# Performance work log

Measured on AMD Instinct MI355X. Metric: run time of the kernel, lower is better.

The kernel has to match this reference:

```python
import jax, jax.numpy as jnp
import numpy as np

N_ATOMS = 100000
N_BONDS = 200001
ATOM_FDIM = 39
BOND_FDIM = 11
MAX_NB = 6
HIDDEN = 256
DEPTH = 6
N_MOLS = 2000
ATOMS_PER_MOL = N_ATOMS // N_MOLS


def setup_inputs() -> dict:
    key = jax.random.key(0)
    ks = jax.random.split(key, 8)
    fatoms = jax.random.uniform(ks[0], (N_ATOMS, ATOM_FDIM), dtype=jnp.float32)
    fbonds = jax.random.uniform(ks[1], (N_BONDS, ATOM_FDIM + BOND_FDIM), dtype=jnp.float32)
    agraph = jax.random.randint(ks[2], (N_ATOMS, MAX_NB), 0, N_BONDS, dtype=jnp.int32)
    bgraph = jax.random.randint(ks[3], (N_BONDS, MAX_NB), 0, N_BONDS, dtype=jnp.int32)
    starts = jnp.arange(N_MOLS, dtype=jnp.int32) * ATOMS_PER_MOL
    scope = jnp.stack([starts, jnp.full((N_MOLS,), ATOMS_PER_MOL, jnp.int32)], axis=1)
    s = 1.0 / np.sqrt(HIDDEN)
    W_i = jax.random.normal(ks[4], (HIDDEN, ATOM_FDIM + BOND_FDIM), dtype=jnp.float32) * s
    W_h = jax.random.normal(ks[5], (HIDDEN, HIDDEN), dtype=jnp.float32) * s
    W_o = jax.random.normal(ks[6], (HIDDEN, ATOM_FDIM + HIDDEN), dtype=jnp.float32) * s
    b_o = jax.random.normal(ks[7], (HIDDEN,), dtype=jnp.float32) * s
    return {"fatoms": fatoms, "fbonds": fbonds, "agraph": agraph,
            "bgraph": bgraph, "scope": scope, "W_i": W_i, "W_h": W_h,
            "W_o": W_o, "b_o": b_o}


def reference(fatoms, fbonds, agraph, bgraph, scope, W_i, W_h, W_o, b_o):
    # Initial bond messages: Linear (no bias) + ReLU
    binput = fbonds @ W_i.T                      # [B_bonds, H]
    message = jax.nn.relu(binput)
    # depth-1 rounds of gather -> sum over MAX_NB neighbors -> Linear -> ReLU + residual
    for _ in range(DEPTH - 1):
        nei = message[bgraph].sum(axis=1)        # [B_bonds, H]
        message = jax.nn.relu(binput + nei @ W_h.T)
    # Atom readout
    nei = message[agraph].sum(axis=1)            # [N_atoms, H]
    ainput = jnp.concatenate([fatoms, nei], axis=1)
    atom_hiddens = jax.nn.relu(ainput @ W_o.T + b_o)
    # Scope mean pooling: equal-size contiguous segments -> reshape-mean
    n_mols = scope.shape[0]
    mol_vecs = atom_hiddens.reshape(n_mols, -1, atom_hiddens.shape[-1]).mean(axis=1)
    return mol_vecs
```

## Files before the change

### kernel.cpp

```cpp
#include <hip/hip_runtime.h>
#include <hip/hip_bf16.h>

#define NB 200001
#define NA 100000
#define HID 256
#define AF 39
#define BFD 50
#define MAXNB 6
#define NMOL 2000
#define APM 50
#define KPAD 320
#define BM 64

typedef __attribute__((ext_vector_type(8))) unsigned short ushort8;
typedef __attribute__((ext_vector_type(8))) short short8;
typedef __attribute__((ext_vector_type(4))) unsigned short u16x4;
typedef __attribute__((ext_vector_type(4))) float f32x4;

__device__ __forceinline__ unsigned short f2b(float f) {
  __hip_bfloat16 h = __float2bfloat16(f);
  return *reinterpret_cast<unsigned short*>(&h);
}
__device__ __forceinline__ float b2f(unsigned short u) {
  union { unsigned int i; float f; } v; v.i = ((unsigned int)u) << 16; return v.f;
}

__global__ void prep_wc(const float* __restrict__ Wi, const float* __restrict__ Wh,
                        unsigned short* __restrict__ WcB) {
  int i = blockIdx.x * 256 + threadIdx.x;
  if (i >= HID * KPAD) return;
  int n = i / KPAD, k = i % KPAD;
  float v = 0.f;
  if (k < BFD) v = Wi[n * BFD + k];
  else if (k >= 64) v = Wh[n * HID + (k - 64)];
  WcB[i] = f2b(v);
}
__global__ void prep_wo(const float* __restrict__ Wo, unsigned short* __restrict__ WoP) {
  int i = blockIdx.x * 256 + threadIdx.x;
  if (i >= HID * KPAD) return;
  int n = i / KPAD, k = i % KPAD;
  float v = 0.f;
  if (k < AF) v = Wo[n * (AF + HID) + k];
  else if (k >= 64) v = Wo[n * (AF + HID) + AF + (k - 64)];
  WoP[i] = f2b(v);
}
__global__ void prep_fb(const float* __restrict__ fbonds, unsigned short* __restrict__ fbpad) {
  int i = blockIdx.x * 256 + threadIdx.x;
  if (i >= NB * 8) return;
  const int bond = i >> 3;
  const int c0 = (i & 7) * 8;
  ushort8 o;
  #pragma unroll
  for (int e = 0; e < 8; ++e) {
    const int c = c0 + e;
    o[e] = f2b(c < BFD ? fbonds[(size_t)bond * BFD + c] : 0.f);
  }
  *reinterpret_cast<ushort8*>(fbpad + (size_t)bond * 64 + c0) = o;
}

template <bool PREPPED>
__device__ __forceinline__ void stage_feat64(unsigned short (*As)[KPAD], int t, int b0,
                                             int nrows_total,
                                             const float* __restrict__ f32src, int f32dim, int realdim,
                                             const unsigned short* __restrict__ padsrc) {
  const int rs = t >> 3, csl = t & 7;
  #pragma unroll
  for (int it = 0; it < 2; ++it) {
    const int r = it * 32 + rs;
    const int row = b0 + r;
    const int c0 = csl * 8;
    ushort8 o;
    #pragma unroll
    for (int e = 0; e < 8; ++e) o[e] = 0;
    if (PREPPED) {
      if (row < nrows_total) o = *reinterpret_cast<const ushort8*>(padsrc + (size_t)row * 64 + c0);
    } else {
      #pragma unroll
      for (int e = 0; e < 8; ++e) {
        const int c = c0 + e;
        if (row < nrows_total && c < realdim) o[e] = f2b(f32src[(size_t)row * f32dim + c]);
      }
    }
    *reinterpret_cast<ushort8*>(&As[r][c0 ^ ((r & 7) << 3)]) = o;
  }
}

#define GLOAD(dst, ROW)                                                              \
  {                                                                                  \
    const int bond_ = b0 + (ROW);                                                    \
    const int* bg_ = graph + (size_t)(bond_ < nrows_total ? bond_ : 0) * MAXNB;      \
    _Pragma("unroll")                                                                \
    for (int j = 0; j < MAXNB; ++j)                                                  \
      dst[j] = *reinterpret_cast<const u16x4*>(msg_in + (size_t)bg_[j] * HID + c0);  \
  }
#define GCONSUME(src, ROW)                                                           \
  {                                                                                  \
    float acc_[4] = {0.f, 0.f, 0.f, 0.f};                                            \
    _Pragma("unroll")                                                                \
    for (int j = 0; j < MAXNB; ++j) {                                                \
      _Pragma("unroll")                                                              \
      for (int e = 0; e < 4; ++e) acc_[e] += b2f(src[j][e]);                         \
    }                                                                                \
    u16x4 o_;                                                                        \
    _Pragma("unroll")                                                                \
    for (int e = 0; e < 4; ++e) o_[e] = f2b(acc_[e]);                                \
    const int r_ = (ROW);                                                            \
    const int cc_ = 64 + c0;                                                         \
    *reinterpret_cast<u16x4*>(&As[r_][cc_ ^ ((r_ & 7) << 3)]) = o_;                  \
  }

__device__ __forceinline__ void gather_rows64(unsigned short (*As)[KPAD],
                                              const int* __restrict__ graph,
                                              int t, int b0, int nrows_total,
                                              const unsigned short* __restrict__ msg_in) {
  const int w = t >> 6;
  const int lane = t & 63;
  const int c0 = lane * 4;
  u16x4 va[MAXNB], vb[MAXNB], vc[MAXNB], vd[MAXNB];
  GLOAD(va, 0 * 4 + w);
  GLOAD(vb, 1 * 4 + w);
  GLOAD(vc, 2 * 4 + w);
  #pragma unroll
  for (int i4 = 0; i4 < 16; i4 += 4) {
    { const int it = i4 + 0; if (it + 3 < 16) GLOAD(vd, (it + 3) * 4 + w); GCONSUME(va, it * 4 + w); }
    { const int it = i4 + 1; if (it + 3 < 16) GLOAD(va, (it + 3) * 4 + w); GCONSUME(vb, it * 4 + w); }
    { const int it = i4 + 2; if (it + 3 < 16) GLOAD(vb, (it + 3) * 4 + w); GCONSUME(vc, it * 4 + w); }
    { const int it = i4 + 3; if (it + 3 < 16) GLOAD(vc, (it + 3) * 4 + w); GCONSUME(vd, it * 4 + w); }
  }
}

template <bool PREPPED>
__global__ __launch_bounds__(256, 4) void init_kernel(
    const float* __restrict__ fbonds, const unsigned short* __restrict__ fbpad,
    const unsigned short* __restrict__ WcB, unsigned short* __restrict__ msg0) {
  __shared__ unsigned short As[BM][KPAD];
  const int t = threadIdx.x;
  const int b0 = blockIdx.x * BM;

  stage_feat64<PREPPED>(As, t, b0, NB, fbonds, BFD, BFD, fbpad);
  __syncthreads();

  const int w = t >> 6, lane = t & 63, lr = lane & 15, lg = lane >> 4;
  f32x4 acc[4][4];
  #pragma unroll
  for (int i = 0; i < 4; ++i)
    #pragma unroll
    for (int j = 0; j < 4; ++j) acc[i][j] = f32x4{0.f, 0.f, 0.f, 0.f};

  const unsigned short* wb[4];
  #pragma unroll
  for (int fn = 0; fn < 4; ++fn) wb[fn] = WcB + (size_t)(w * 64 + fn * 16 + lr) * KPAD;

  #pragma unroll
  for (int ks = 0; ks < 2; ++ks) {
    const int kb = ks * 32 + lg * 8;
    short8 a[4], b[4];
    #pragma unroll
    for (int fm = 0; fm < 4; ++fm) {
      const int m = fm * 16 + lr;
      a[fm] = *reinterpret_cast<const short8*>(&As[m][kb ^ ((m & 7) << 3)]);
    }
    #pragma unroll
    for (int fn = 0; fn < 4; ++fn)
      b[fn] = *reinterpret_cast<const short8*>(wb[fn] + kb);
    #pragma unroll
    for (int fm = 0; fm < 4; ++fm)
      #pragma unroll
      for (int fn = 0; fn < 4; ++fn)
        acc[fm][fn] = __builtin_amdgcn_mfma_f32_16x16x32_bf16(a[fm], b[fn], acc[fm][fn], 0, 0, 0);
  }

  #pragma unroll
  for (int fm = 0; fm < 4; ++fm)
    #pragma unroll
    for (int r = 0; r < 4; ++r) {
      const int m = fm * 16 + lg * 4 + r;
      const int bond = b0 + m;
      if (bond < NB) {
        #pragma unroll
        for (int fn = 0; fn < 4; ++fn) {
          const int col = w * 64 + fn * 16 + lr;
          msg0[(size_t)bond * HID + col] = f2b(fmaxf(acc[fm][fn][r], 0.f));
        }
      }
    }
}

template <bool PREPPED>
__global__ __launch_bounds__(256, 4) void round_kernel(
    const unsigned short* __restrict__ msg_in, unsigned short* __restrict__ msg_out,
    const float* __restrict__ fbonds, const unsigned short* __restrict__ fbpad,
    const unsigned short* __restrict__ WcB, const int* __restrict__ bgraph) {
  __shared__ unsigned short As[BM][KPAD];
  const int t = threadIdx.x;
  const int b0 = blockIdx.x * BM;

  stage_feat64<PREPPED>(As, t, b0, NB, fbonds, BFD, BFD, fbpad);
  gather_rows64(As, bgraph, t, b0, NB, msg_in);
  __syncthreads();

  const int w = t >> 6, lane = t & 63, lr = lane & 15, lg = lane >> 4;
  f32x4 acc[4][4];
  #pragma unroll
  for (int i = 0; i < 4; ++i)
    #pragma unroll
    for (int j = 0; j < 4; ++j) acc[i][j] = f32x4{0.f, 0.f, 0.f, 0.f};

  const unsigned short* wb[4];
  #pragma unroll
  for (int fn = 0; fn < 4; ++fn) wb[fn] = WcB + (size_t)(w * 64 + fn * 16 + lr) * KPAD;

  for (int kstep = 0; kstep < 5; ++kstep) {
    #pragma unroll
    for (int ks = 0; ks < 2; ++ks) {
      const int kb = ks * 32 + lg * 8;
      const int kA = kstep * 64 + kb;
      short8 a[4], b[4];
      #pragma unroll
      for (int fm = 0; fm < 4; ++fm) {
        const int m = fm * 16 + lr;
        a[fm] = *reinterpret_cast<const short8*>(&As[m][kA ^ ((m & 7) << 3)]);
      }
      #pragma unroll
      for (int fn = 0; fn < 4; ++fn)
        b[fn] = *reinterpret_cast<const short8*>(wb[fn] + kstep * 64 + kb);
      #pragma unroll
      for (int fm = 0; fm < 4; ++fm)
        #pragma unroll
        for (int fn = 0; fn < 4; ++fn)
          acc[fm][fn] = __builtin_amdgcn_mfma_f32_16x16x32_bf16(a[fm], b[fn], acc[fm][fn], 0, 0, 0);
    }
  }

  #pragma unroll
  for (int fm = 0; fm < 4; ++fm)
    #pragma unroll
    for (int r = 0; r < 4; ++r) {
      const int m = fm * 16 + lg * 4 + r;
      const int bond = b0 + m;
      if (bond < NB) {
        #pragma unroll
        for (int fn = 0; fn < 4; ++fn) {
          const int col = w * 64 + fn * 16 + lr;
          __builtin_nontemporal_store(f2b(fmaxf(acc[fm][fn][r], 0.f)),
                                      &msg_out[(size_t)bond * HID + col]);
        }
      }
    }
}

__global__ __launch_bounds__(256, 4) void readout_kernel(
    const unsigned short* __restrict__ msg_in, const float* __restrict__ fatoms,
    const unsigned short* __restrict__ WoP, const float* __restrict__ b_o,
    const int* __restrict__ agraph, float* __restrict__ atomh) {
  __shared__ unsigned short As[BM][KPAD];
  const int t = threadIdx.x;
  const int a0 = blockIdx.x * BM;

  stage_feat64<false>(As, t, a0, NA, fatoms, AF, AF, nullptr);
  gather_rows64(As, agraph, t, a0, NA, msg_in);
  __syncthreads();

  const int w = t >> 6, lane = t & 63, lr = lane & 15, lg = lane >> 4;
  f32x4 acc[4][4];
  #pragma unroll
  for (int i = 0; i < 4; ++i)
    #pragma unroll
    for (int j = 0; j < 4; ++j) acc[i][j] = f32x4{0.f, 0.f, 0.f, 0.f};

  const unsigned short* wb[4];
  #pragma unroll
  for (int fn = 0; fn < 4; ++fn) wb[fn] = WoP + (size_t)(w * 64 + fn * 16 + lr) * KPAD;

  for (int kstep = 0; kstep < 5; ++kstep) {
    #pragma unroll
    for (int ks = 0; ks < 2; ++ks) {
      const int kb = ks * 32 + lg * 8;
      const int kA = kstep * 64 + kb;
      short8 a[4], b[4];
      #pragma unroll
      for (int fm = 0; fm < 4; ++fm) {
        const int m = fm * 16 + lr;
        a[fm] = *reinterpret_cast<const short8*>(&As[m][kA ^ ((m & 7) << 3)]);
      }
      #pragma unroll
      for (int fn = 0; fn < 4; ++fn)
        b[fn] = *reinterpret_cast<const short8*>(wb[fn] + kstep * 64 + kb);
      #pragma unroll
      for (int fm = 0; fm < 4; ++fm)
        #pragma unroll
        for (int fn = 0; fn < 4; ++fn)
          acc[fm][fn] = __builtin_amdgcn_mfma_f32_16x16x32_bf16(a[fm], b[fn], acc[fm][fn], 0, 0, 0);
    }
  }

  #pragma unroll
  for (int fm = 0; fm < 4; ++fm)
    #pragma unroll
    for (int r = 0; r < 4; ++r) {
      const int m = fm * 16 + lg * 4 + r;
      const int atom = a0 + m;
      if (atom < NA) {
        #pragma unroll
        for (int fn = 0; fn < 4; ++fn) {
          const int col = w * 64 + fn * 16 + lr;
          const float v = acc[fm][fn][r] + b_o[col];
          __builtin_nontemporal_store(fmaxf(v, 0.f), &atomh[(size_t)atom * HID + col]);
        }
      }
    }
}

__global__ __launch_bounds__(256) void pool_kernel(const float* __restrict__ atomh,
                                                   float* __restrict__ out) {
  const int mol = blockIdx.x;
  const int t = threadIdx.x;
  const float* base = atomh + (size_t)mol * APM * HID + t;
  float s = 0.f;
  #pragma unroll 5
  for (int i = 0; i < APM; ++i) s += base[(size_t)i * HID];
  out[(size_t)mol * HID + t] = s * (1.f / APM);
}

extern "C" void kernel_launch(void* const* d_in, const int* in_sizes, int n_in,
                              void* d_out, int out_size, void* d_ws, size_t ws_size,
                              hipStream_t stream) {
  const float* fatoms = (const float*)d_in[0];
  const float* fbonds = (const float*)d_in[1];
  const int* agraph = (const int*)d_in[2];
  const int* bgraph = (const int*)d_in[3];
  const float* W_i = (const float*)d_in[5];
  const float* W_h = (const float*)d_in[6];
  const float* W_o = (const float*)d_in[7];
  const float* b_o = (const float*)d_in[8];

  char* ws = (char*)d_ws;
  size_t off = 0;
  auto alloc = [&](size_t bytes) {
    void* p = ws + off;
    off += (bytes + 255) & ~(size_t)255;
    return p;
  };
  unsigned short* msgA = (unsigned short*)alloc((size_t)NB * HID * 2);
  unsigned short* msgB = (unsigned short*)alloc((size_t)NB * HID * 2);
  unsigned short* WcB = (unsigned short*)alloc((size_t)HID * KPAD * 2);
  unsigned short* WoP = (unsigned short*)alloc((size_t)HID * KPAD * 2);
  const size_t base_need = off;
  unsigned short* fbpad = (unsigned short*)alloc((size_t)NB * 64 * 2);
  const size_t fb_need = off;
  float* atomh = (float*)msgA;

  if (ws_size < base_need) return;
  const bool prepped = (ws_size >= fb_need);

  prep_wc<<<(HID * KPAD + 255) / 256, 256, 0, stream>>>(W_i, W_h, WcB);
  prep_wo<<<(HID * KPAD + 255) / 256, 256, 0, stream>>>(W_o, WoP);
  if (prepped)
    prep_fb<<<(NB * 8 + 255) / 256, 256, 0, stream>>>(fbonds, fbpad);

  const int nblk_b = (NB + BM - 1) / BM;
  if (prepped)
    init_kernel<true><<<nblk_b, 256, 0, stream>>>(fbonds, fbpad, WcB, msgA);
  else
    init_kernel<false><<<nblk_b, 256, 0, stream>>>(fbonds, fbpad, WcB, msgA);

  unsigned short* src = msgA;
  unsigned short* dst = msgB;
  for (int d = 0; d < 5; ++d) {
    if (prepped)
      round_kernel<true><<<nblk_b, 256, 0, stream>>>(src, dst, fbonds, fbpad, WcB, bgraph);
    else
      round_kernel<false><<<nblk_b, 256, 0, stream>>>(src, dst, fbonds, fbpad, WcB, bgraph);
    unsigned short* tmp = src; src = dst; dst = tmp;
  }

  const int nblk_a = (NA + BM - 1) / BM;
  readout_kernel<<<nblk_a, 256, 0, stream>>>(src, fatoms, WoP, b_o, agraph, atomh);
  pool_kernel<<<NMOL, 256, 0, stream>>>(atomh, (float*)d_out);
}
```

Measured before the change: 959.1 us.

## Quantize bond messages to 8-bit with per-row scales to halve gather traffic

Stores each round's bond messages as unsigned 8-bit values with a per-bond float scale instead of bf16. The GEMM epilogue now does a cross-wave row max through shared memory to compute the scale. Gathers dequantize on the fly, halving the bytes pulled by the random-access neighbour gather that dominates each round. This adds extra syncs and reductions in the epilogue and loses precision relative to bf16. The workspace layout also changes: fbpad now aliases the atomh buffer and the unprepped fallback path is removed.

```diff
diff --git a/kernel.cpp b/kernel.cpp
--- a/kernel.cpp
+++ b/kernel.cpp
@@ -58,10 +58,8 @@
   *reinterpret_cast<ushort8*>(fbpad + (size_t)bond * 64 + c0) = o;
 }
 
-template <bool PREPPED>
 __device__ __forceinline__ void stage_feat64(unsigned short (*As)[KPAD], int t, int b0,
                                              int nrows_total,
-                                             const float* __restrict__ f32src, int f32dim, int realdim,
                                              const unsigned short* __restrict__ padsrc) {
   const int rs = t >> 3, csl = t & 7;
   #pragma unroll
@@ -72,72 +70,135 @@
     ushort8 o;
     #pragma unroll
     for (int e = 0; e < 8; ++e) o[e] = 0;
-    if (PREPPED) {
-      if (row < nrows_total) o = *reinterpret_cast<const ushort8*>(padsrc + (size_t)row * 64 + c0);
-    } else {
-      #pragma unroll
-      for (int e = 0; e < 8; ++e) {
-        const int c = c0 + e;
-        if (row < nrows_total && c < realdim) o[e] = f2b(f32src[(size_t)row * f32dim + c]);
-      }
-    }
+    if (row < nrows_total) o = *reinterpret_cast<const ushort8*>(padsrc + (size_t)row * 64 + c0);
     *reinterpret_cast<ushort8*>(&As[r][c0 ^ ((r & 7) << 3)]) = o;
   }
 }
-
-#define GLOAD(dst, ROW)                                                              \
+__device__ __forceinline__ void stage_feat64_f32(unsigned short (*As)[KPAD], int t, int b0,
+                                                 int nrows_total,
+                                                 const float* __restrict__ f32src, int f32dim,
+                                                 int realdim) {
+  const int rs = t >> 3, csl = t & 7;
+  #pragma unroll
+  for (int it = 0; it < 2; ++it) {
+    const int r = it * 32 + rs;
+    const int row = b0 + r;
+    const int c0 = csl * 8;
+    ushort8 o;
+    #pragma unroll
+    for (int e = 0; e < 8; ++e) o[e] = 0;
+    #pragma unroll
+    for (int e = 0; e < 8; ++e) {
+      const int c = c0 + e;
+      if (row < nrows_total && c < realdim) o[e] = f2b(f32src[(size_t)row * f32dim + c]);
+    }
+    *reinterpret_cast<ushort8*>(&As[r][c0 ^ ((r & 7) << 3)]) = o;
+  }
+}
+
+#define GLOAD(dst, dsc, ROW)                                                         \
   {                                                                                  \
     const int bond_ = b0 + (ROW);                                                    \
     const int* bg_ = graph + (size_t)(bond_ < nrows_total ? bond_ : 0) * MAXNB;      \
     _Pragma("unroll")                                                                \
-    for (int j = 0; j < MAXNB; ++j)                                                  \
-      dst[j] = *reinterpret_cast<const u16x4*>(msg_in + (size_t)bg_[j] * HID + c0);  \
-  }
-#define GCONSUME(src, ROW)                                                           \
+    for (int j = 0; j < MAXNB; ++j) {                                                \
+      const int nb_ = bg_[j];                                                        \
+      dst[j] = msg32[(size_t)nb_ * (HID / 4) + lane];                                \
+      dsc[j] = scl_in[nb_];                                                          \
+    }                                                                                \
+  }
+#define GCONSUME(src, ssc, ROW)                                                      \
   {                                                                                  \
-    float acc_[4] = {0.f, 0.f, 0.f, 0.f};                                            \
+    float a0 = 0.f, a1 = 0.f, a2 = 0.f, a3 = 0.f;                                    \
     _Pragma("unroll")                                                                \
     for (int j = 0; j < MAXNB; ++j) {                                                \
-      _Pragma("unroll")                                                              \
-      for (int e = 0; e < 4; ++e) acc_[e] += b2f(src[j][e]);                         \
+      const unsigned int d_ = src[j];                                                \
+      const float s_ = ssc[j];                                                       \
+      a0 += (float)(d_ & 0xffu) * s_;                                                \
+      a1 += (float)((d_ >> 8) & 0xffu) * s_;                                         \
+      a2 += (float)((d_ >> 16) & 0xffu) * s_;                                        \
+      a3 += (float)(d_ >> 24) * s_;                                                  \
     }                                                                                \
     u16x4 o_;                                                                        \
-    _Pragma("unroll")                                                                \
-    for (int e = 0; e < 4; ++e) o_[e] = f2b(acc_[e]);                                \
+    o_[0] = f2b(a0); o_[1] = f2b(a1); o_[2] = f2b(a2); o_[3] = f2b(a3);              \
     const int r_ = (ROW);                                                            \
     const int cc_ = 64 + c0;                                                         \
     *reinterpret_cast<u16x4*>(&As[r_][cc_ ^ ((r_ & 7) << 3)]) = o_;                  \
   }
 
-__device__ __forceinline__ void gather_rows64(unsigned short (*As)[KPAD],
-                                              const int* __restrict__ graph,
-                                              int t, int b0, int nrows_total,
-                                              const unsigned short* __restrict__ msg_in) {
+__device__ __forceinline__ void gather_rows64_q8(unsigned short (*As)[KPAD],
+                                                 const int* __restrict__ graph,
+                                                 int t, int b0, int nrows_total,
+                                                 const unsigned int* __restrict__ msg32,
+                                                 const float* __restrict__ scl_in) {
   const int w = t >> 6;
   const int lane = t & 63;
   const int c0 = lane * 4;
-  u16x4 va[MAXNB], vb[MAXNB], vc[MAXNB], vd[MAXNB];
-  GLOAD(va, 0 * 4 + w);
-  GLOAD(vb, 1 * 4 + w);
-  GLOAD(vc, 2 * 4 + w);
+  unsigned int va[MAXNB], vb[MAXNB], vc[MAXNB], vd[MAXNB];
+  float sa[MAXNB], sb[MAXNB], sc[MAXNB], sd[MAXNB];
+  GLOAD(va, sa, 0 * 4 + w);
+  GLOAD(vb, sb, 1 * 4 + w);
+  GLOAD(vc, sc, 2 * 4 + w);
   #pragma unroll
   for (int i4 = 0; i4 < 16; i4 += 4) {
-    { const int it = i4 + 0; if (it + 3 < 16) GLOAD(vd, (it + 3) * 4 + w); GCONSUME(va, it * 4 + w); }
-    { const int it = i4 + 1; if (it + 3 < 16) GLOAD(va, (it + 3) * 4 + w); GCONSUME(vb, it * 4 + w); }
-    { const int it = i4 + 2; if (it + 3 < 16) GLOAD(vb, (it + 3) * 4 + w); GCONSUME(vc, it * 4 + w); }
-    { const int it = i4 + 3; if (it + 3 < 16) GLOAD(vc, (it + 3) * 4 + w); GCONSUME(vd, it * 4 + w); }
-  }
-}
-
-template <bool PREPPED>
+    { const int it = i4 + 0; if (it + 3 < 16) GLOAD(vd, sd, (it + 3) * 4 + w); GCONSUME(va, sa, it * 4 + w); }
+    { const int it = i4 + 1; if (it + 3 < 16) GLOAD(va, sa, (it + 3) * 4 + w); GCONSUME(vb, sb, it * 4 + w); }
+    { const int it = i4 + 2; if (it + 3 < 16) GLOAD(vb, sb, (it + 3) * 4 + w); GCONSUME(vc, sc, it * 4 + w); }
+    { const int it = i4 + 3; if (it + 3 < 16) GLOAD(vc, sc, (it + 3) * 4 + w); GCONSUME(vd, sd, it * 4 + w); }
+  }
+}
+
+__device__ __forceinline__ void quant_store(f32x4 (&acc)[4][4], unsigned short (*As)[KPAD],
+                                            int t, int b0,
+                                            unsigned char* __restrict__ msg_out,
+                                            float* __restrict__ scale_out) {
+  const int w = t >> 6, lane = t & 63, lr = lane & 15, lg = lane >> 4;
+  float* wls = reinterpret_cast<float*>(As);
+  __syncthreads();
+  #pragma unroll
+  for (int fm = 0; fm < 4; ++fm)
+    #pragma unroll
+    for (int r = 0; r < 4; ++r) {
+      float mx = 0.f;
+      #pragma unroll
+      for (int fn = 0; fn < 4; ++fn) mx = fmaxf(mx, acc[fm][fn][r]);
+      #pragma unroll
+      for (int s = 1; s < 16; s <<= 1) mx = fmaxf(mx, __shfl_xor(mx, s));
+      if (lr == 0) wls[(fm * 16 + lg * 4 + r) * 4 + w] = mx;
+    }
+  __syncthreads();
+  #pragma unroll
+  for (int fm = 0; fm < 4; ++fm)
+    #pragma unroll
+    for (int r = 0; r < 4; ++r) {
+      const int m = fm * 16 + lg * 4 + r;
+      const int bond = b0 + m;
+      const float mx = fmaxf(fmaxf(wls[m * 4 + 0], wls[m * 4 + 1]),
+                             fmaxf(wls[m * 4 + 2], wls[m * 4 + 3]));
+      const float scl = mx * (1.f / 255.f);
+      const float inv = mx > 0.f ? 255.f / mx : 0.f;
+      if (bond < NB) {
+        if (w == 0 && lr == 0) scale_out[bond] = scl;
+        #pragma unroll
+        for (int fn = 0; fn < 4; ++fn) {
+          const int col = w * 64 + fn * 16 + lr;
+          const float v = fmaxf(acc[fm][fn][r], 0.f);
+          int q = __float2int_rn(v * inv);
+          q = q > 255 ? 255 : q;
+          msg_out[(size_t)bond * HID + col] = (unsigned char)q;
+        }
+      }
+    }
+}
+
 __global__ __launch_bounds__(256, 4) void init_kernel(
-    const float* __restrict__ fbonds, const unsigned short* __restrict__ fbpad,
-    const unsigned short* __restrict__ WcB, unsigned short* __restrict__ msg0) {
+    const unsigned short* __restrict__ fbpad, const unsigned short* __restrict__ WcB,
+    unsigned char* __restrict__ msg0, float* __restrict__ scale0) {
   __shared__ unsigned short As[BM][KPAD];
   const int t = threadIdx.x;
   const int b0 = blockIdx.x * BM;
 
-  stage_feat64<PREPPED>(As, t, b0, NB, fbonds, BFD, BFD, fbpad);
+  stage_feat64(As, t, b0, NB, fbpad);
   __syncthreads();
 
   const int w = t >> 6, lane = t & 63, lr = lane & 15, lg = lane >> 4;
@@ -170,33 +231,20 @@
         acc[fm][fn] = __builtin_amdgcn_mfma_f32_16x16x32_bf16(a[fm], b[fn], acc[fm][fn], 0, 0, 0);
   }
 
-  #pragma unroll
-  for (int fm = 0; fm < 4; ++fm)
-    #pragma unroll
-    for (int r = 0; r < 4; ++r) {
-      const int m = fm * 16 + lg * 4 + r;
-      const int bond = b0 + m;
-      if (bond < NB) {
-        #pragma unroll
-        for (int fn = 0; fn < 4; ++fn) {
-          const int col = w * 64 + fn * 16 + lr;
-          msg0[(size_t)bond * HID + col] = f2b(fmaxf(acc[fm][fn][r], 0.f));
-        }
-      }
-    }
-}
-
-template <bool PREPPED>
+  quant_store(acc, As, t, b0, msg0, scale0);
+}
+
 __global__ __launch_bounds__(256, 4) void round_kernel(
-    const unsigned short* __restrict__ msg_in, unsigned short* __restrict__ msg_out,
-    const float* __restrict__ fbonds, const unsigned short* __restrict__ fbpad,
-    const unsigned short* __restrict__ WcB, const int* __restrict__ bgraph) {
+    const unsigned int* __restrict__ msg_in32, const float* __restrict__ scale_in,
+    unsigned char* __restrict__ msg_out, float* __restrict__ scale_out,
+    const unsigned short* __restrict__ fbpad, const unsigned short* __restrict__ WcB,
+    const int* __restrict__ bgraph) {
   __shared__ unsigned short As[BM][KPAD];
   const int t = threadIdx.x;
   const int b0 = blockIdx.x * BM;
 
-  stage_feat64<PREPPED>(As, t, b0, NB, fbonds, BFD, BFD, fbpad);
-  gather_rows64(As, bgraph, t, b0, NB, msg_in);
+  stage_feat64(As, t, b0, NB, fbpad);
+  gather_rows64_q8(As, bgraph, t, b0, NB, msg_in32, scale_in);
   __syncthreads();
 
   const int w = t >> 6, lane = t & 63, lr = lane & 15, lg = lane >> 4;
@@ -232,33 +280,20 @@
     }
   }
 
-  #pragma unroll
-  for (int fm = 0; fm < 4; ++fm)
-    #pragma unroll
-    for (int r = 0; r < 4; ++r) {
-      const int m = fm * 16 + lg * 4 + r;
-      const int bond = b0 + m;
-      if (bond < NB) {
-        #pragma unroll
-        for (int fn = 0; fn < 4; ++fn) {
-          const int col = w * 64 + fn * 16 + lr;
-          __builtin_nontemporal_store(f2b(fmaxf(acc[fm][fn][r], 0.f)),
-                                      &msg_out[(size_t)bond * HID + col]);
-        }
-      }
-    }
+  quant_store(acc, As, t, b0, msg_out, scale_out);
 }
 
 __global__ __launch_bounds__(256, 4) void readout_kernel(
-    const unsigned short* __restrict__ msg_in, const float* __restrict__ fatoms,
-    const unsigned short* __restrict__ WoP, const float* __restrict__ b_o,
-    const int* __restrict__ agraph, float* __restrict__ atomh) {
+    const unsigned int* __restrict__ msg_in32, const float* __restrict__ scale_in,
+    const float* __restrict__ fatoms, const unsigned short* __restrict__ WoP,
+    const float* __restrict__ b_o, const int* __restrict__ agraph,
+    float* __restrict__ atomh) {
   __shared__ unsigned short As[BM][KPAD];
   const int t = threadIdx.x;
   const int a0 = blockIdx.x * BM;
 
-  stage_feat64<false>(As, t, a0, NA, fatoms, AF, AF, nullptr);
-  gather_rows64(As, agraph, t, a0, NA, msg_in);
+  stage_feat64_f32(As, t, a0, NA, fatoms, AF, AF);
+  gather_rows64_q8(As, agraph, t, a0, NA, msg_in32, scale_in);
   __syncthreads();
 
   const int w = t >> 6, lane = t & 63, lr = lane & 15, lg = lane >> 4;
@@ -305,7 +340,7 @@
         for (int fn = 0; fn < 4; ++fn) {
           const int col = w * 64 + fn * 16 + lr;
           const float v = acc[fm][fn][r] + b_o[col];
-          __builtin_nontemporal_store(fmaxf(v, 0.f), &atomh[(size_t)atom * HID + col]);
+          atomh[(size_t)atom * HID + col] = fmaxf(v, 0.f);
         }
       }
     }
@@ -341,40 +376,36 @@
     off += (bytes + 255) & ~(size_t)255;
     return p;
   };
-  unsigned short* msgA = (unsigned short*)alloc((size_t)NB * HID * 2);
-  unsigned short* msgB = (unsigned short*)alloc((size_t)NB * HID * 2);
+  unsigned char* msgA = (unsigned char*)alloc((size_t)NB * HID);
+  unsigned char* msgB = (unsigned char*)alloc((size_t)NB * HID);
+  float* sclA = (float*)alloc((size_t)NB * 4);
+  float* sclB = (float*)alloc((size_t)NB * 4);
   unsigned short* WcB = (unsigned short*)alloc((size_t)HID * KPAD * 2);
   unsigned short* WoP = (unsigned short*)alloc((size_t)HID * KPAD * 2);
-  const size_t base_need = off;
-  unsigned short* fbpad = (unsigned short*)alloc((size_t)NB * 64 * 2);
-  const size_t fb_need = off;
-  float* atomh = (float*)msgA;
-
-  if (ws_size < base_need) return;
-  const bool prepped = (ws_size >= fb_need);
+  float* atomh = (float*)alloc((size_t)NA * HID * 4);
+  unsigned short* fbpad = (unsigned short*)atomh;
+  const size_t need = off;
+
+  if (ws_size < need) return;
 
   prep_wc<<<(HID * KPAD + 255) / 256, 256, 0, stream>>>(W_i, W_h, WcB);
   prep_wo<<<(HID * KPAD + 255) / 256, 256, 0, stream>>>(W_o, WoP);
-  if (prepped)
-    prep_fb<<<(NB * 8 + 255) / 256, 256, 0, stream>>>(fbonds, fbpad);
+  prep_fb<<<(NB * 8 + 255) / 256, 256, 0, stream>>>(fbonds, fbpad);
 
   const int nblk_b = (NB + BM - 1) / BM;
-  if (prepped)
-    init_kernel<true><<<nblk_b, 256, 0, stream>>>(fbonds, fbpad, WcB, msgA);
-  else
-    init_kernel<false><<<nblk_b, 256, 0, stream>>>(fbonds, fbpad, WcB, msgA);
-
-  unsigned short* src = msgA;
-  unsigned short* dst = msgB;
+  init_kernel<<<nblk_b, 256, 0, stream>>>(fbpad, WcB, msgA, sclA);
+
+  unsigned char* src = msgA;  float* ssrc = sclA;
+  unsigned char* dst = msgB;  float* sdst = sclB;
   for (int d = 0; d < 5; ++d) {
-    if (prepped)
-      round_kernel<true><<<nblk_b, 256, 0, stream>>>(src, dst, fbonds, fbpad, WcB, bgraph);
-    else
-      round_kernel<false><<<nblk_b, 256, 0, stream>>>(src, dst, fbonds, fbpad, WcB, bgraph);
-    unsigned short* tmp = src; src = dst; dst = tmp;
+    round_kernel<<<nblk_b, 256, 0, stream>>>((const unsigned int*)src, ssrc, dst, sdst,
+                                             fbpad, WcB, bgraph);
+    unsigned char* tm = src; src = dst; dst = tm;
+    float* ts = ssrc; ssrc = sdst; sdst = ts;
   }
 
   const int nblk_a = (NA + BM - 1) / BM;
-  readout_kernel<<<nblk_a, 256, 0, stream>>>(src, fatoms, WoP, b_o, agraph, atomh);
+  readout_kernel<<<nblk_a, 256, 0, stream>>>((const unsigned int*)src, ssrc, fatoms, WoP,
+                                             b_o, agraph, atomh);
   pool_kernel<<<NMOL, 256, 0, stream>>>(atomh, (float*)d_out);
 }
```

After: 821.9 us. 1.17x faster.
